# Kernel optimization log

Hardware: AMD Instinct MI355X
Metric: run time of the kernel (lower is better)

Reference implementation:

```python
import jax, jax.numpy as jnp
import numpy as np


def setup_inputs() -> dict:
    key = jax.random.key(0)
    k1, k2 = jax.random.split(key)
    B, S, N, D = 4, 8, 2048, 3
    pred_points = jax.random.normal(k1, (B, S, N, D), dtype=jnp.float32)
    target_points = jax.random.normal(k2, (B, S, N, D), dtype=jnp.float32)
    return {"pred_points": pred_points, "target_points": target_points}


def reference(pred_points, target_points):
    # pred_points, target_points: [B, S, N, 3]
    seq_len = pred_points.shape[1]
    # Pairwise Euclidean distances via the GEMM identity |p-t|^2 = |p|^2 + |t|^2 - 2 p.t
    p2 = jnp.sum(pred_points * pred_points, axis=-1)      # [B,S,N]
    t2 = jnp.sum(target_points * target_points, axis=-1)  # [B,S,M]
    cross = jnp.einsum('bsnd,bsmd->bsnm', pred_points, target_points)  # [B,S,N,M]
    d2 = p2[..., :, None] + t2[..., None, :] - 2.0 * cross
    d = jnp.sqrt(jnp.maximum(d2, 0.0))  # [B,S,N,M]
    # Bidirectional nearest-neighbor min + mean over points
    min_p2t = jnp.min(d, axis=3)  # [B,S,N]
    min_t2p = jnp.min(d, axis=2)  # [B,S,M]
    chamfer = jnp.mean(min_p2t, axis=2) + jnp.mean(min_t2p, axis=2)  # [B,S]
    total_loss = jnp.sum(chamfer, axis=1)  # [B] (sum over timesteps)
    # reduction == 'mean'
    return jnp.mean(total_loss) / seq_len
```

## Files before the change

kernel.cpp:

```cpp
#include <hip/hip_runtime.h>
#include <math.h>

#define N_PTS   2048
#define BLOCK   128
#define NQ      16
#define SLAB    64
#define NSLAB   (N_PTS / SLAB)

__global__ __launch_bounds__(BLOCK, 4) void chamfer_min_kernel(
    const float* __restrict__ pred,
    const float* __restrict__ tgt,
    unsigned int* __restrict__ wsmin,
    float* __restrict__ out)
{
    __shared__ float4 sh[SLAB];

    const int bs   = blockIdx.x;
    const int dir  = blockIdx.y;
    const int slab = blockIdx.z;
    const int tid  = threadIdx.x;

    if (bs == 0 && dir == 0 && slab == 0 && tid == 0)
        atomicExch((unsigned int*)out, 0u);

    const float* Abase = (dir ? tgt : pred) + (size_t)bs * N_PTS * 3;
    const float* Bbase = (dir ? pred : tgt) + (size_t)bs * N_PTS * 3;

    if (tid < SLAB) {
        const int j = slab * SLAB + tid;
        const float x = Bbase[3 * j + 0];
        const float y = Bbase[3 * j + 1];
        const float z = Bbase[3 * j + 2];
        sh[tid] = make_float4(x, y, z, x * x + y * y + z * z);
    }

    float nx[NQ], ny[NQ], nz[NQ], p2[NQ], best[NQ];
    #pragma unroll
    for (int k = 0; k < NQ; ++k) {
        const int q = tid + BLOCK * k;
        const float px = Abase[3 * q + 0];
        const float py = Abase[3 * q + 1];
        const float pz = Abase[3 * q + 2];
        nx[k] = -2.0f * px;
        ny[k] = -2.0f * py;
        nz[k] = -2.0f * pz;
        p2[k] = px * px + py * py + pz * pz;
        best[k] = 3.4e38f;
    }
    __syncthreads();

    #pragma unroll 4
    for (int j = 0; j < SLAB; j += 2) {
        const float4 t0 = sh[j];
        const float4 t1 = sh[j + 1];
        #pragma unroll
        for (int k = 0; k < NQ; ++k) {
            const float v0 = fmaf(nx[k], t0.x,
                             fmaf(ny[k], t0.y,
                             fmaf(nz[k], t0.z, t0.w)));
            const float v1 = fmaf(nx[k], t1.x,
                             fmaf(ny[k], t1.y,
                             fmaf(nz[k], t1.z, t1.w)));
            best[k] = fminf(fminf(best[k], v0), v1);
        }
    }

    const int base = (dir * 32 + bs) * N_PTS;
    #pragma unroll
    for (int k = 0; k < NQ; ++k) {
        const float d2 = fmaxf(p2[k] + best[k], 0.0f);
        atomicMin(&wsmin[base + tid + BLOCK * k], __float_as_uint(d2));
    }
}

__global__ __launch_bounds__(256) void chamfer_finalize_kernel(
    const float4* __restrict__ wsmin,
    float* __restrict__ out)
{
    __shared__ float red[256 / 64];
    const int i = blockIdx.x * 256 + threadIdx.x;
    const float4 t = wsmin[i];
    float s = sqrtf(t.x) + sqrtf(t.y) + sqrtf(t.z) + sqrtf(t.w);

    for (int off = 32; off > 0; off >>= 1)
        s += __shfl_down(s, off, 64);
    const int tid = threadIdx.x;
    if ((tid & 63) == 0) red[tid >> 6] = s;
    __syncthreads();
    if (tid == 0) {
        const float blk = red[0] + red[1] + red[2] + red[3];
        atomicAdd(out, blk * (1.0f / 65536.0f));
    }
}

extern "C" void kernel_launch(void* const* d_in, const int* in_sizes, int n_in,
                              void* d_out, int out_size, void* d_ws, size_t ws_size,
                              hipStream_t stream) {
    const float* pred = (const float*)d_in[0];
    const float* tgt  = (const float*)d_in[1];
    float* out = (float*)d_out;
    unsigned int* wsmin = (unsigned int*)d_ws;

    hipMemsetAsync(wsmin, 0x7F, (size_t)131072 * sizeof(unsigned int), stream);

    dim3 grid(32, 2, NSLAB);
    chamfer_min_kernel<<<grid, BLOCK, 0, stream>>>(pred, tgt, wsmin, out);

    chamfer_finalize_kernel<<<131072 / (256 * 4), 256, 0, stream>>>(
        (const float4*)wsmin, out);
}
```

Measured before the change: 83.58 us.

## Read target slab via uniform global loads instead of LDS, widen block

Drops the shared-memory staging and __syncthreads, so each thread reads the target slab straight from global memory with warp-uniform addresses (likely scalar loads) and recomputes |t|^2 inline. Block size goes to 256 with 8 queries per thread and the slab to 128 points, which halves the grid's slab count and so the number of atomicMin passes. The risk is global load latency inside the inner loop, extra per-point norm work repeated in every wave, and fewer queries per thread to amortize each target load.

```diff
diff --git a/kernel.cpp b/kernel.cpp
--- a/kernel.cpp
+++ b/kernel.cpp
@@ -2,19 +2,17 @@
 #include <math.h>
 
 #define N_PTS   2048
-#define BLOCK   128
-#define NQ      16
-#define SLAB    64
+#define BLOCK   256
+#define NQ      8
+#define SLAB    128
 #define NSLAB   (N_PTS / SLAB)
 
-__global__ __launch_bounds__(BLOCK, 4) void chamfer_min_kernel(
+__global__ __launch_bounds__(BLOCK) void chamfer_min_kernel(
     const float* __restrict__ pred,
     const float* __restrict__ tgt,
     unsigned int* __restrict__ wsmin,
     float* __restrict__ out)
 {
-    __shared__ float4 sh[SLAB];
-
     const int bs   = blockIdx.x;
     const int dir  = blockIdx.y;
     const int slab = blockIdx.z;
@@ -24,15 +22,8 @@
         atomicExch((unsigned int*)out, 0u);
 
     const float* Abase = (dir ? tgt : pred) + (size_t)bs * N_PTS * 3;
-    const float* Bbase = (dir ? pred : tgt) + (size_t)bs * N_PTS * 3;
-
-    if (tid < SLAB) {
-        const int j = slab * SLAB + tid;
-        const float x = Bbase[3 * j + 0];
-        const float y = Bbase[3 * j + 1];
-        const float z = Bbase[3 * j + 2];
-        sh[tid] = make_float4(x, y, z, x * x + y * y + z * z);
-    }
+    const float* Bbase = (dir ? pred : tgt) + (size_t)bs * N_PTS * 3
+                         + (size_t)slab * SLAB * 3;
 
     float nx[NQ], ny[NQ], nz[NQ], p2[NQ], best[NQ];
     #pragma unroll
@@ -47,20 +38,25 @@
         p2[k] = px * px + py * py + pz * pz;
         best[k] = 3.4e38f;
     }
-    __syncthreads();
 
     #pragma unroll 4
     for (int j = 0; j < SLAB; j += 2) {
-        const float4 t0 = sh[j];
-        const float4 t1 = sh[j + 1];
+        const float x0 = Bbase[3 * j + 0];
+        const float y0 = Bbase[3 * j + 1];
+        const float z0 = Bbase[3 * j + 2];
+        const float x1 = Bbase[3 * j + 3];
+        const float y1 = Bbase[3 * j + 4];
+        const float z1 = Bbase[3 * j + 5];
+        const float w0 = x0 * x0 + y0 * y0 + z0 * z0;
+        const float w1 = x1 * x1 + y1 * y1 + z1 * z1;
         #pragma unroll
         for (int k = 0; k < NQ; ++k) {
-            const float v0 = fmaf(nx[k], t0.x,
-                             fmaf(ny[k], t0.y,
-                             fmaf(nz[k], t0.z, t0.w)));
-            const float v1 = fmaf(nx[k], t1.x,
-                             fmaf(ny[k], t1.y,
-                             fmaf(nz[k], t1.z, t1.w)));
+            const float v0 = fmaf(nx[k], x0,
+                             fmaf(ny[k], y0,
+                             fmaf(nz[k], z0, w0)));
+            const float v1 = fmaf(nx[k], x1,
+                             fmaf(ny[k], y1,
+                             fmaf(nz[k], z1, w1)));
             best[k] = fminf(fminf(best[k], v0), v1);
         }
     }
```

New measurement: 87.89 us. 5.2% more time.
